# Performance work log

Measured on AMD Instinct MI355X. Metric: run time of the kernel, lower is better.

The kernel has to match this reference:

```python
import jax, jax.numpy as jnp
import numpy as np

H, W = 256, 256
N = 1024          # num gaussians
K = 4             # num clusters
M = 50            # num components
ALPHA_THRESH = 1.0 / 255.0
ALPHA_CLAMP = 0.999


def setup_inputs() -> dict:
    key = jax.random.key(0)
    k1, k2, k3 = jax.random.split(key, 3)
    # torch init: atanh(2*(rand-0.5)); keep away from +-1 for finite atanh
    u = jax.random.uniform(k1, (N, 2), minval=0.01, maxval=0.99)
    xyz_raw = jnp.arctanh(2.0 * (u - 0.5))
    cholesky_raw = jax.random.uniform(k2, (N, 3))
    opacity = jnp.ones((N, 1), jnp.float32)
    features_dc = jax.random.uniform(k3, (K, M, N, 3))
    return {"xyz_raw": xyz_raw, "cholesky_raw": cholesky_raw,
            "opacity": opacity, "features_dc": features_dc, "cluster_id": 0}


def _gaussian_weights(xyz_raw, cholesky_raw, opacity):
    """Dense equivalent of project_gaussians_2d + rasterize_gaussians_sum weights.
    Returns [H*W, N] per-pixel per-gaussian alpha."""
    xy = jnp.tanh(xyz_raw)                                  # [N,2] in (-1,1)
    chol = cholesky_raw + jnp.array([0.5, 0.0, 0.5], dtype=cholesky_raw.dtype)
    l1, l2, l3 = chol[:, 0], chol[:, 1], chol[:, 2]
    # cov = L L^T with L = [[l1,0],[l2,l3]]
    a = l1 * l1
    b = l1 * l2
    c = l2 * l2 + l3 * l3
    det = a * c - b * b
    conic1, conic2, conic3 = c / det, -b / det, a / det      # inverse covariance
    # ndc -> pixel centers (gsplat ndc2pix convention)
    cx = 0.5 * ((xy[:, 0] + 1.0) * W - 1.0)                  # [N]
    cy = 0.5 * ((xy[:, 1] + 1.0) * H - 1.0)
    px = jnp.arange(W, dtype=xyz_raw.dtype)
    py = jnp.arange(H, dtype=xyz_raw.dtype)
    pxf = jnp.tile(px, H)                                    # [H*W] x coord
    pyf = jnp.repeat(py, W)                                  # [H*W] y coord
    dx = cx[None, :] - pxf[:, None]                          # [H*W, N]
    dy = cy[None, :] - pyf[:, None]
    sigma = 0.5 * (conic1[None, :] * dx * dx + conic3[None, :] * dy * dy) \
            + conic2[None, :] * dx * dy
    alpha = jnp.minimum(ALPHA_CLAMP, opacity[:, 0][None, :] * jnp.exp(-sigma))
    valid = (sigma >= 0.0) & (alpha >= ALPHA_THRESH)
    return jnp.where(valid, alpha, 0.0)                      # [H*W, N]


def reference(xyz_raw, cholesky_raw, opacity, features_dc, cluster_id):
    wgt = _gaussian_weights(xyz_raw, cholesky_raw, opacity)  # [H*W, N]
    feats = features_dc[cluster_id]                          # [M, N, 3]
    # out_stack[m,c,h,w] = sum_n wgt[p,n] * feats[m,n,c]  (background=0, scale=1, shift=0)
    out = jnp.einsum('pn,mnc->mcp', wgt, feats)
    return out.reshape(M, 3, H, W)
```

## Files before the change

### kernel.cpp

```cpp
#include <hip/hip_runtime.h>
#include <hip/hip_bf16.h>


namespace {
constexpr int WID = 256, HEI = 256, NPIX = WID * HEI;
constexpr int NG = 1024;
constexpr int MREP = 50;
constexpr int MC = 150;
constexpr int MCCHUNK = 25;
constexpr int ZCH = 6;
constexpr int TLX = 64, TLY = 4;
constexpr int CCAP = 64;
constexpr int FP = 28;
}

struct GParam { float cx, cy, A, B, C3, op, rx, ry; };

__device__ __forceinline__ float ldf(const void* p, int i, bool isb) {
    if (isb) return __bfloat162float(((const __hip_bfloat16*)p)[i]);
    return ((const float*)p)[i];
}

__device__ __forceinline__ GParam compute_gparam(const void* xyz, const void* chol,
                                                 const void* opac, int n, bool isb) {
    GParam g;
    float l1 = ldf(chol, 3 * n + 0, isb) + 0.5f;
    float l2 = ldf(chol, 3 * n + 1, isb);
    float l3 = ldf(chol, 3 * n + 2, isb) + 0.5f;
    float a = l1 * l1;
    float b = l1 * l2;
    float c = l2 * l2 + l3 * l3;
    float det = a * c - b * b;
    float inv = 1.0f / det;
    g.A = c * inv;
    g.B = -b * inv;
    g.C3 = a * inv;
    float x0 = tanhf(ldf(xyz, 2 * n + 0, isb));
    float x1 = tanhf(ldf(xyz, 2 * n + 1, isb));
    g.cx = 0.5f * ((x0 + 1.0f) * (float)WID - 1.0f);
    g.cy = 0.5f * ((x1 + 1.0f) * (float)HEI - 1.0f);
    g.op = ldf(opac, n, isb);
    float smax = logf(255.0f * g.op);
    if (smax > 0.0f) {
        g.rx = sqrtf(2.0f * smax * a) + 0.5f;
        g.ry = sqrtf(2.0f * smax * c) + 0.5f;
    } else {
        g.rx = -1.0f;
        g.ry = -1.0f;
    }
    return g;
}

__global__ __launch_bounds__(256) void prep_kernel(const void* __restrict__ xyz,
                                                   const void* __restrict__ chol,
                                                   const void* __restrict__ opac,
                                                   GParam* __restrict__ gp) {
    int n = blockIdx.x * 256 + threadIdx.x;
    if (n >= NG) return;
    bool isb = (((const unsigned*)opac)[0] == 0x3F803F80u);
    gp[n] = compute_gparam(xyz, chol, opac, n, isb);
}

template <bool HASGP>
__global__ __launch_bounds__(256) void raster_kernel(const GParam* __restrict__ gp,
                                                     const void* __restrict__ xyz,
                                                     const void* __restrict__ chol,
                                                     const void* __restrict__ opac,
                                                     const void* __restrict__ feats,
                                                     const int* __restrict__ cluster,
                                                     void* __restrict__ out) {
    __shared__ unsigned short cand[NG];
    __shared__ int candCnt;
    __shared__ float pLDS[CCAP][8];
    __shared__ float featLDS[CCAP * FP];

    const bool isb = (((const unsigned*)opac)[0] == 0x3F803F80u);
    const int tid = threadIdx.x;
    const int tx0 = blockIdx.x * TLX;
    const int ty0 = blockIdx.y * TLY;
    const int mc0 = blockIdx.z * MCCHUNK;

    if (tid == 0) candCnt = 0;
    __syncthreads();

    for (int g = tid; g < NG; g += 256) {
        GParam gg = HASGP ? gp[g] : compute_gparam(xyz, chol, opac, g, isb);
        bool keep = (gg.rx >= 0.0f) &&
                    (gg.cx + gg.rx >= (float)tx0) && (gg.cx - gg.rx <= (float)(tx0 + TLX - 1)) &&
                    (gg.cy + gg.ry >= (float)ty0) && (gg.cy - gg.ry <= (float)(ty0 + TLY - 1));
        if (keep) {
            int slot = atomicAdd(&candCnt, 1);
            cand[slot] = (unsigned short)g;
        }
    }
    __syncthreads();
    const int C = candCnt;

    const int clus = cluster[0];
    const int fbase = clus * (MREP * NG * 3);
    const int lx = tid & 63, ly = tid >> 6;
    const float px = (float)(tx0 + lx);
    const float py = (float)(ty0 + ly);

    float acc[FP];
#pragma unroll
    for (int q = 0; q < FP; ++q) acc[q] = 0.0f;

    for (int base = 0; base < C; base += CCAP) {
        const int nStage = (C - base < CCAP) ? (C - base) : CCAP;
        __syncthreads();
        if (tid < nStage) {
            int n = cand[base + tid];
            GParam gg = HASGP ? gp[n] : compute_gparam(xyz, chol, opac, n, isb);
            pLDS[tid][0] = gg.cx;
            pLDS[tid][1] = gg.cy;
            pLDS[tid][2] = gg.A;
            pLDS[tid][3] = gg.B;
            pLDS[tid][4] = gg.C3;
            pLDS[tid][5] = gg.op;
            pLDS[tid][6] = gg.ry;
            pLDS[tid][7] = 0.0f;
        }
        for (int t = tid; t < nStage * FP; t += 256) {
            int il = t / FP;
            int q = t - il * FP;
            float v = 0.0f;
            if (q < MCCHUNK) {
                int mc = mc0 + q;
                int m = mc / 3, cch = mc - m * 3;
                int n = cand[base + il];
                v = ldf(feats, fbase + m * (NG * 3) + n * 3 + cch, isb);
            }
            featLDS[t] = v;
        }
        __syncthreads();

        for (int jb = 0; jb < nStage; jb += 4) {
            const int nj = nStage - jb;
            float amv[4] = {0.0f, 0.0f, 0.0f, 0.0f};
#pragma unroll
            for (int k = 0; k < 4; ++k) {
                if (k < nj) {
                    const float4* p4 = (const float4*)&pLDS[jb + k][0];
                    float4 u = p4[0], v = p4[1];
                    float dx = u.x - px;
                    float dy = u.y - py;
                    float sig = 0.5f * (u.z * dx * dx + v.x * dy * dy) + u.w * dx * dy;
                    float al = fminf(0.999f, v.y * __expf(-sig));
                    bool valid = (sig >= 0.0f) && (al >= (1.0f / 255.0f));
                    amv[k] = valid ? al : 0.0f;
                }
            }
#pragma unroll
            for (int k = 0; k < 4; ++k) {
                if (k < nj && __any(amv[k] != 0.0f)) {
                    const float am = amv[k];
                    const float4* f4 = (const float4*)&featLDS[(jb + k) * FP];
#pragma unroll
                    for (int q4 = 0; q4 < FP / 4; ++q4) {
                        float4 f = f4[q4];
                        acc[4 * q4 + 0] += am * f.x;
                        acc[4 * q4 + 1] += am * f.y;
                        acc[4 * q4 + 2] += am * f.z;
                        acc[4 * q4 + 3] += am * f.w;
                    }
                }
            }
        }
    }

    const int pix = (ty0 + ly) * WID + tx0 + lx;
    if (isb) {
        __hip_bfloat16* o = (__hip_bfloat16*)out;
#pragma unroll
        for (int q = 0; q < MCCHUNK; ++q) o[(mc0 + q) * NPIX + pix] = __float2bfloat16(acc[q]);
    } else {
        float* o = (float*)out;
#pragma unroll
        for (int q = 0; q < MCCHUNK; ++q) o[(mc0 + q) * NPIX + pix] = acc[q];
    }
}

extern "C" void kernel_launch(void* const* d_in, const int* in_sizes, int n_in,
                              void* d_out, int out_size, void* d_ws, size_t ws_size,
                              hipStream_t stream) {
    const void* xyz = d_in[0];
    const void* chol = d_in[1];
    const void* opac = d_in[2];
    const void* feats = d_in[3];
    const int* cl = (const int*)d_in[4];
    (void)in_sizes; (void)n_in; (void)out_size;

    const bool hasgp = (ws_size >= NG * sizeof(GParam));
    GParam* gp = hasgp ? (GParam*)d_ws : nullptr;
    if (hasgp) {
        prep_kernel<<<dim3((NG + 255) / 256), 256, 0, stream>>>(xyz, chol, opac, gp);
    }
    dim3 grid(WID / TLX, HEI / TLY, ZCH);
    if (hasgp) {
        raster_kernel<true><<<grid, 256, 0, stream>>>(gp, xyz, chol, opac, feats, cl, d_out);
    } else {
        raster_kernel<false><<<grid, 256, 0, stream>>>(gp, xyz, chol, opac, feats, cl, d_out);
    }
}
```

Baseline: 87.93 us.

## Precompute per-tile cull lists and transposed features, drop LDS staging in raster

Adds prep kernels that transpose the selected cluster's features into a per-gaussian, chunk-contiguous workspace layout and build per-tile candidate lists once, instead of culling all 1024 gaussians in each of the six z-chunk blocks. The raster kernel then walks the tile list with wave-uniform (readfirstlane) indices, reading params and features from global/scalar memory directly with no LDS staging or barriers. This costs three extra launches and scalar-memory latency per gaussian, and falls back to a full scan when a tile exceeds the list capacity.

Measured after the change: 90.54 us. 3.0% more time.

```diff
diff --git a/kernel.cpp b/kernel.cpp
--- a/kernel.cpp
+++ b/kernel.cpp
@@ -10,8 +10,16 @@
 constexpr int MCCHUNK = 25;
 constexpr int ZCH = 6;
 constexpr int TLX = 64, TLY = 4;
-constexpr int CCAP = 64;
+constexpr int NTX = WID / TLX;
+constexpr int NTILE = NTX * (HEI / TLY);
+constexpr int TCAP = 96;
 constexpr int FP = 28;
+constexpr int FSTR = ZCH * FP;
+constexpr size_t WS_GP = 0;
+constexpr size_t WS_FEAT = 32 * 1024;
+constexpr size_t WS_CNT = WS_FEAT + (size_t)NG * FSTR * 4;
+constexpr size_t WS_LIST = WS_CNT + NTILE * 4;
+constexpr size_t WS_TOTAL = WS_LIST + (size_t)NTILE * TCAP * 4;
 }
 
 struct GParam { float cx, cy, A, B, C3, op, rx, ry; };
@@ -19,6 +27,10 @@
 __device__ __forceinline__ float ldf(const void* p, int i, bool isb) {
     if (isb) return __bfloat162float(((const __hip_bfloat16*)p)[i]);
     return ((const float*)p)[i];
+}
+
+__device__ __forceinline__ bool is_bf16(const void* opac) {
+    return ((const unsigned*)opac)[0] == 0x3F803F80u;
 }
 
 __device__ __forceinline__ GParam compute_gparam(const void* xyz, const void* chol,
@@ -51,120 +63,173 @@
     return g;
 }
 
-__global__ __launch_bounds__(256) void prep_kernel(const void* __restrict__ xyz,
+__global__ __launch_bounds__(256) void prep_params(const void* __restrict__ xyz,
                                                    const void* __restrict__ chol,
                                                    const void* __restrict__ opac,
                                                    GParam* __restrict__ gp) {
     int n = blockIdx.x * 256 + threadIdx.x;
     if (n >= NG) return;
-    bool isb = (((const unsigned*)opac)[0] == 0x3F803F80u);
-    gp[n] = compute_gparam(xyz, chol, opac, n, isb);
-}
-
-template <bool HASGP>
-__global__ __launch_bounds__(256) void raster_kernel(const GParam* __restrict__ gp,
-                                                     const void* __restrict__ xyz,
-                                                     const void* __restrict__ chol,
-                                                     const void* __restrict__ opac,
-                                                     const void* __restrict__ feats,
-                                                     const int* __restrict__ cluster,
-                                                     void* __restrict__ out) {
+    gp[n] = compute_gparam(xyz, chol, opac, n, is_bf16(opac));
+}
+
+__global__ __launch_bounds__(256) void prep_feat(const void* __restrict__ feats,
+                                                 const void* __restrict__ opac,
+                                                 const int* __restrict__ cluster,
+                                                 float* __restrict__ featT) {
+    int idx = blockIdx.x * 256 + threadIdx.x;
+    if (idx >= NG * MC) return;
+    bool isb = is_bf16(opac);
+    int n = idx / MC;
+    int mc = idx - n * MC;
+    int z = mc / MCCHUNK, r = mc - z * MCCHUNK;
+    int m = mc / 3, cch = mc - m * 3;
+    int fbase = cluster[0] * (MREP * NG * 3);
+    featT[n * FSTR + z * FP + r] = ldf(feats, fbase + m * (NG * 3) + n * 3 + cch, isb);
+}
+
+__global__ __launch_bounds__(256) void cull_kernel(const GParam* __restrict__ gp,
+                                                   int* __restrict__ tileCnt,
+                                                   int* __restrict__ tileList) {
+    const int tile = blockIdx.x;
+    const float x0 = (float)((tile & (NTX - 1)) * TLX);
+    const float y0 = (float)((tile >> 2) * TLY);
+    const float x1 = x0 + (float)(TLX - 1);
+    const float y1 = y0 + (float)(TLY - 1);
+    __shared__ int cnt;
+    if (threadIdx.x == 0) cnt = 0;
+    __syncthreads();
+    for (int g = threadIdx.x; g < NG; g += 256) {
+        GParam gg = gp[g];
+        bool keep = (gg.rx >= 0.0f) &&
+                    (gg.cx + gg.rx >= x0) && (gg.cx - gg.rx <= x1) &&
+                    (gg.cy + gg.ry >= y0) && (gg.cy - gg.ry <= y1);
+        if (keep) {
+            int s = atomicAdd(&cnt, 1);
+            if (s < TCAP) tileList[tile * TCAP + s] = g;
+        }
+    }
+    __syncthreads();
+    if (threadIdx.x == 0) tileCnt[tile] = cnt;
+}
+
+__global__ __launch_bounds__(256) void raster_ws(const GParam* __restrict__ gp,
+                                                 const float* __restrict__ featT,
+                                                 const int* __restrict__ tileCnt,
+                                                 const int* __restrict__ tileList,
+                                                 const void* __restrict__ opac,
+                                                 void* __restrict__ out) {
+    const bool isb = is_bf16(opac);
+    const int tid = threadIdx.x;
+    const int lx = tid & 63, ly = tid >> 6;
+    const int tx0 = blockIdx.x * TLX;
+    const int ty0 = blockIdx.y * TLY;
+    const int z = blockIdx.z;
+    const int tile = blockIdx.y * NTX + blockIdx.x;
+    const float px = (float)(tx0 + lx);
+    const float py = (float)(ty0 + ly);
+
+    float acc[MCCHUNK];
+#pragma unroll
+    for (int q = 0; q < MCCHUNK; ++q) acc[q] = 0.0f;
+
+    const int cnt = __builtin_amdgcn_readfirstlane(tileCnt[tile]);
+
+    auto process = [&](int n) {
+        GParam g = gp[n];
+        float dx = g.cx - px;
+        float dy = g.cy - py;
+        float sig = 0.5f * (g.A * dx * dx + g.C3 * dy * dy) + g.B * dx * dy;
+        float al = fminf(0.999f, g.op * __expf(-sig));
+        float am = (sig >= 0.0f && al >= (1.0f / 255.0f)) ? al : 0.0f;
+        if (__any(am != 0.0f)) {
+            const float* f = featT + n * FSTR + z * FP;
+#pragma unroll
+            for (int q = 0; q < MCCHUNK; ++q) acc[q] += am * f[q];
+        }
+    };
+
+    if (cnt <= TCAP) {
+        for (int j = 0; j < cnt; ++j) {
+            int n = __builtin_amdgcn_readfirstlane(tileList[tile * TCAP + j]);
+            process(n);
+        }
+    } else {
+        const float x0 = (float)tx0, y0 = (float)ty0;
+        const float x1 = x0 + (float)(TLX - 1), y1 = y0 + (float)(TLY - 1);
+        for (int n = 0; n < NG; ++n) {
+            GParam gg = gp[n];
+            bool keep = (gg.rx >= 0.0f) &&
+                        (gg.cx + gg.rx >= x0) && (gg.cx - gg.rx <= x1) &&
+                        (gg.cy + gg.ry >= y0) && (gg.cy - gg.ry <= y1);
+            if (keep) process(n);
+        }
+    }
+
+    const int pix = (ty0 + ly) * WID + tx0 + lx;
+    const int mc0 = z * MCCHUNK;
+    if (isb) {
+        __hip_bfloat16* o = (__hip_bfloat16*)out;
+#pragma unroll
+        for (int q = 0; q < MCCHUNK; ++q) o[(mc0 + q) * NPIX + pix] = __float2bfloat16(acc[q]);
+    } else {
+        float* o = (float*)out;
+#pragma unroll
+        for (int q = 0; q < MCCHUNK; ++q) o[(mc0 + q) * NPIX + pix] = acc[q];
+    }
+}
+
+__global__ __launch_bounds__(256) void raster_nows(const void* __restrict__ xyz,
+                                                   const void* __restrict__ chol,
+                                                   const void* __restrict__ opac,
+                                                   const void* __restrict__ feats,
+                                                   const int* __restrict__ cluster,
+                                                   void* __restrict__ out) {
     __shared__ unsigned short cand[NG];
     __shared__ int candCnt;
-    __shared__ float pLDS[CCAP][8];
-    __shared__ float featLDS[CCAP * FP];
-
-    const bool isb = (((const unsigned*)opac)[0] == 0x3F803F80u);
+    const bool isb = is_bf16(opac);
     const int tid = threadIdx.x;
+    const int lx = tid & 63, ly = tid >> 6;
     const int tx0 = blockIdx.x * TLX;
     const int ty0 = blockIdx.y * TLY;
-    const int mc0 = blockIdx.z * MCCHUNK;
+    const int z = blockIdx.z;
+    const int mc0 = z * MCCHUNK;
+    const float px = (float)(tx0 + lx);
+    const float py = (float)(ty0 + ly);
+    const int fbase = cluster[0] * (MREP * NG * 3);
 
     if (tid == 0) candCnt = 0;
     __syncthreads();
-
     for (int g = tid; g < NG; g += 256) {
-        GParam gg = HASGP ? gp[g] : compute_gparam(xyz, chol, opac, g, isb);
+        GParam gg = compute_gparam(xyz, chol, opac, g, isb);
         bool keep = (gg.rx >= 0.0f) &&
                     (gg.cx + gg.rx >= (float)tx0) && (gg.cx - gg.rx <= (float)(tx0 + TLX - 1)) &&
                     (gg.cy + gg.ry >= (float)ty0) && (gg.cy - gg.ry <= (float)(ty0 + TLY - 1));
         if (keep) {
-            int slot = atomicAdd(&candCnt, 1);
-            cand[slot] = (unsigned short)g;
+            int s = atomicAdd(&candCnt, 1);
+            cand[s] = (unsigned short)g;
         }
     }
     __syncthreads();
     const int C = candCnt;
 
-    const int clus = cluster[0];
-    const int fbase = clus * (MREP * NG * 3);
-    const int lx = tid & 63, ly = tid >> 6;
-    const float px = (float)(tx0 + lx);
-    const float py = (float)(ty0 + ly);
-
-    float acc[FP];
-#pragma unroll
-    for (int q = 0; q < FP; ++q) acc[q] = 0.0f;
-
-    for (int base = 0; base < C; base += CCAP) {
-        const int nStage = (C - base < CCAP) ? (C - base) : CCAP;
-        __syncthreads();
-        if (tid < nStage) {
-            int n = cand[base + tid];
-            GParam gg = HASGP ? gp[n] : compute_gparam(xyz, chol, opac, n, isb);
-            pLDS[tid][0] = gg.cx;
-            pLDS[tid][1] = gg.cy;
-            pLDS[tid][2] = gg.A;
-            pLDS[tid][3] = gg.B;
-            pLDS[tid][4] = gg.C3;
-            pLDS[tid][5] = gg.op;
-            pLDS[tid][6] = gg.ry;
-            pLDS[tid][7] = 0.0f;
-        }
-        for (int t = tid; t < nStage * FP; t += 256) {
-            int il = t / FP;
-            int q = t - il * FP;
-            float v = 0.0f;
-            if (q < MCCHUNK) {
+    float acc[MCCHUNK];
+#pragma unroll
+    for (int q = 0; q < MCCHUNK; ++q) acc[q] = 0.0f;
+
+    for (int j = 0; j < C; ++j) {
+        int n = __builtin_amdgcn_readfirstlane((int)cand[j]);
+        GParam g = compute_gparam(xyz, chol, opac, n, isb);
+        float dx = g.cx - px;
+        float dy = g.cy - py;
+        float sig = 0.5f * (g.A * dx * dx + g.C3 * dy * dy) + g.B * dx * dy;
+        float al = fminf(0.999f, g.op * __expf(-sig));
+        float am = (sig >= 0.0f && al >= (1.0f / 255.0f)) ? al : 0.0f;
+        if (__any(am != 0.0f)) {
+#pragma unroll
+            for (int q = 0; q < MCCHUNK; ++q) {
                 int mc = mc0 + q;
                 int m = mc / 3, cch = mc - m * 3;
-                int n = cand[base + il];
-                v = ldf(feats, fbase + m * (NG * 3) + n * 3 + cch, isb);
-            }
-            featLDS[t] = v;
-        }
-        __syncthreads();
-
-        for (int jb = 0; jb < nStage; jb += 4) {
-            const int nj = nStage - jb;
-            float amv[4] = {0.0f, 0.0f, 0.0f, 0.0f};
-#pragma unroll
-            for (int k = 0; k < 4; ++k) {
-                if (k < nj) {
-                    const float4* p4 = (const float4*)&pLDS[jb + k][0];
-                    float4 u = p4[0], v = p4[1];
-                    float dx = u.x - px;
-                    float dy = u.y - py;
-                    float sig = 0.5f * (u.z * dx * dx + v.x * dy * dy) + u.w * dx * dy;
-                    float al = fminf(0.999f, v.y * __expf(-sig));
-                    bool valid = (sig >= 0.0f) && (al >= (1.0f / 255.0f));
-                    amv[k] = valid ? al : 0.0f;
-                }
-            }
-#pragma unroll
-            for (int k = 0; k < 4; ++k) {
-                if (k < nj && __any(amv[k] != 0.0f)) {
-                    const float am = amv[k];
-                    const float4* f4 = (const float4*)&featLDS[(jb + k) * FP];
-#pragma unroll
-                    for (int q4 = 0; q4 < FP / 4; ++q4) {
-                        float4 f = f4[q4];
-                        acc[4 * q4 + 0] += am * f.x;
-                        acc[4 * q4 + 1] += am * f.y;
-                        acc[4 * q4 + 2] += am * f.z;
-                        acc[4 * q4 + 3] += am * f.w;
-                    }
-                }
+                acc[q] += am * ldf(feats, fbase + m * (NG * 3) + n * 3 + cch, isb);
             }
         }
     }
@@ -191,15 +256,18 @@
     const int* cl = (const int*)d_in[4];
     (void)in_sizes; (void)n_in; (void)out_size;
 
-    const bool hasgp = (ws_size >= NG * sizeof(GParam));
-    GParam* gp = hasgp ? (GParam*)d_ws : nullptr;
-    if (hasgp) {
-        prep_kernel<<<dim3((NG + 255) / 256), 256, 0, stream>>>(xyz, chol, opac, gp);
-    }
     dim3 grid(WID / TLX, HEI / TLY, ZCH);
-    if (hasgp) {
-        raster_kernel<true><<<grid, 256, 0, stream>>>(gp, xyz, chol, opac, feats, cl, d_out);
-    } else {
-        raster_kernel<false><<<grid, 256, 0, stream>>>(gp, xyz, chol, opac, feats, cl, d_out);
-    }
-}
+    if (ws_size >= WS_TOTAL) {
+        char* ws = (char*)d_ws;
+        GParam* gp = (GParam*)(ws + WS_GP);
+        float* featT = (float*)(ws + WS_FEAT);
+        int* tileCnt = (int*)(ws + WS_CNT);
+        int* tileList = (int*)(ws + WS_LIST);
+        prep_params<<<dim3((NG + 255) / 256), 256, 0, stream>>>(xyz, chol, opac, gp);
+        prep_feat<<<dim3((NG * MC + 255) / 256), 256, 0, stream>>>(feats, opac, cl, featT);
+        cull_kernel<<<dim3(NTILE), 256, 0, stream>>>(gp, tileCnt, tileList);
+        raster_ws<<<grid, 256, 0, stream>>>(gp, featT, tileCnt, tileList, opac, d_out);
+    } else {
+        raster_nows<<<grid, 256, 0, stream>>>(xyz, chol, opac, feats, cl, d_out);
+    }
+}
```
